# Performance work log

Measured on AMD Instinct MI355X. Metric: run time of the kernel, lower is better.

Reference implementation:

```python
import jax, jax.numpy as jnp
import numpy as np
from jax import lax

B, S, T = 32, 24, 48           # batch, max_num_strokes, max_stroke_len
ENC, SCH, STH = 512, 512, 512  # enc_dim, scene_hdim, stroke_hdim


def _w(k, shape):
    return (jax.random.normal(k, shape, jnp.float32) / np.sqrt(shape[-1])).astype(jnp.float32)


def setup_inputs() -> dict:
    key = jax.random.key(0)
    ks = jax.random.split(key, 12)
    return {
        "enc_features": jax.random.normal(ks[0], (B, ENC), jnp.float32),
        "vector_sketch": jax.random.normal(ks[1], (B, S, T, 5), jnp.float32),
        # force max length == T and num strokes == S so torch's dynamic .max()
        # bounds coincide with the static shapes used here
        "batch_num_strokes": jnp.full((B, 1), S, jnp.int32),
        "batch_stroke_len": jax.random.randint(ks[2], (B, S), 1, T + 1, jnp.int32).at[0, 0].set(T),
        # scene LSTMCell (input = enc_dim + stroke_hdim), torch gate order i,f,g,o
        "W_sc_ih": _w(ks[3], (4 * SCH, ENC + STH)),
        "W_sc_hh": _w(ks[4], (4 * SCH, SCH)),
        "b_sc": jnp.zeros((4 * SCH,), jnp.float32),  # b_ih + b_hh folded
        # stroke LSTM layer 0 (input = scene_hdim + 5)
        "W0_ih": _w(ks[5], (4 * STH, SCH + 5)),
        "W0_hh": _w(ks[6], (4 * STH, STH)),
        "b0": jnp.zeros((4 * STH,), jnp.float32),
        # stroke LSTM layer 1 (input = stroke_hdim)
        "W1_ih": _w(ks[7], (4 * STH, STH)),
        "W1_hh": _w(ks[8], (4 * STH, STH)),
        "b1": jnp.zeros((4 * STH,), jnp.float32),
        # linear_output: stroke_hdim -> 5
        "W_out": _w(ks[9], (5, STH)),
        "b_out": jnp.zeros((5,), jnp.float32),
    }


def _lstm_cell(x, h, c, Wih, Whh, b):
    g = x @ Wih.T + h @ Whh.T + b
    i, f, gg, o = jnp.split(g, 4, axis=-1)
    c = jax.nn.sigmoid(f) * c + jax.nn.sigmoid(i) * jnp.tanh(gg)
    return jax.nn.sigmoid(o) * jnp.tanh(c), c


def _forward(enc_features, vector_sketch, W_sc_ih, W_sc_hh, b_sc, W0_ih, W0_hh, b0,
             W1_ih, W1_hh, b1, W_out, b_out, batch_stroke_len):
    nb = enc_features.shape[0]
    zs = jnp.zeros((nb, SCH), jnp.float32)
    init_tok0 = jnp.tile(jnp.array([[0., 0., 1., 0., 0.]], jnp.float32), (nb, 1))
    t_idx = jnp.arange(T + 1)

    def stroke_step(carry, xs):
        scene_h, scene_c, prev_tok, init_tok = carry
        sketch_s, lens_s = xs                       # (B,T,5), (B,)
        ctx = jnp.concatenate([enc_features, prev_tok], axis=-1)
        scene_h2, scene_c2 = _lstm_cell(ctx, scene_h, scene_c, W_sc_ih, W_sc_hh, b_sc)
        coords = jnp.concatenate([init_tok[:, None, :], sketch_s], axis=1)  # (B,T+1,5)
        lengths = lens_s + 1                        # pack lengths

        def time_step(c2, xt):
            h0, c0, h1, c1 = c2
            x_t, t = xt
            m = (t < lengths)[:, None]              # packed-sequence validity mask
            h0n, c0n = _lstm_cell(jnp.concatenate([scene_h2, x_t], axis=-1), h0, c0, W0_ih, W0_hh, b0)
            h1n, c1n = _lstm_cell(h0n, h1, c1, W1_ih, W1_hh, b1)
            h0 = jnp.where(m, h0n, h0); c0 = jnp.where(m, c0n, c0)
            h1 = jnp.where(m, h1n, h1); c1 = jnp.where(m, c1n, c1)
            return (h0, c0, h1, c1), jnp.where(m, h1, 0.0)  # pad_packed zero-pads outputs

        z = jnp.zeros((nb, STH), jnp.float32)
        (_, _, h1f, _), outs = lax.scan(time_step, (z, z, z, z), (jnp.swapaxes(coords, 0, 1), t_idx))
        # linear applied AFTER zero-padding, so padded-but-within-L steps get the bias (matches torch)
        out_coords = jnp.swapaxes(outs, 0, 1) @ W_out.T + b_out      # (B,T+1,5)
        L = jnp.max(lens_s)
        valid = (jnp.arange(T) < L)[None, :, None]
        stroke_out = jnp.where(valid, out_coords[:, :T, :], 0.0)     # (B,T,5)
        prev_tok = lax.stop_gradient(h1f)          # .detach() in torch
        last = jnp.clip(lens_s - 1, 0, None)
        init_tok2 = jnp.take_along_axis(sketch_s, last[:, None, None], axis=1)[:, 0, :]
        return (scene_h2, scene_c2, prev_tok, init_tok2), stroke_out

    xs = (jnp.swapaxes(vector_sketch, 0, 1), batch_stroke_len.T)     # (S,B,T,5), (S,B)
    _, outs = lax.scan(stroke_step, (zs, zs, zs, init_tok0), xs)
    return jnp.transpose(outs, (1, 0, 2, 3))       # (B,S,T,5)


def reference(enc_features, vector_sketch, batch_num_strokes, batch_stroke_len,
              W_sc_ih, W_sc_hh, b_sc, W0_ih, W0_hh, b0, W1_ih, W1_hh, b1, W_out, b_out):
    # batch_num_strokes only sets the (static) stroke loop bound S
    del batch_num_strokes
    return _forward(enc_features, vector_sketch, W_sc_ih, W_sc_hh, b_sc, W0_ih, W0_hh,
                    b0, W1_ih, W1_hh, b1, W_out, b_out, batch_stroke_len)
```

## Files before the change

kernel.cpp:

```cpp
#include <hip/hip_runtime.h>

#define NB 256
#define NT 256
#define AGT __HIP_MEMORY_SCOPE_AGENT
typedef unsigned long long ull;
typedef _Float16 f16;
typedef __attribute__((ext_vector_type(8))) _Float16 f16x8;
typedef __attribute__((ext_vector_type(4))) float f32x4;
typedef __attribute__((ext_vector_type(4))) unsigned u32x4;


#define BSTR 1056

struct __align__(16) SMem {
  unsigned short Bt[2][2][4 * 528];
  float X[2][4][8];
  int sLens[2][4];
  int sLmax[2];
};

__device__ __forceinline__ float sigm(float x) { return 1.0f / (1.0f + expf(-x)); }
__device__ __forceinline__ unsigned short f16b(float x) {
  union { _Float16 h; unsigned short u; } q; q.h = (_Float16)x; return q.u;
}
__device__ __forceinline__ ull pk4(float a, float b, float c, float d) {
  union { _Float16 h; unsigned short u; } q;
  ull r; q.h = (_Float16)a; r = q.u; q.h = (_Float16)b; r |= (ull)q.u << 16;
  q.h = (_Float16)c; r |= (ull)q.u << 32; q.h = (_Float16)d; r |= (ull)q.u << 48;
  return r;
}
__device__ __forceinline__ u32x4 ld1x16(const void* p) {
  u32x4 r;
  asm volatile("global_load_dwordx4 %0, %1, off sc0 sc1\ns_waitcnt vmcnt(0)"
               : "=&v"(r) : "v"(p) : "memory");
  return r;
}

extern "C" __global__ void __launch_bounds__(NT, 1)
rnn_decoder_kernel(const float* __restrict__ enc, const float* __restrict__ sketch,
                   const int* __restrict__ slen,
                   const float* __restrict__ Wsc_ih, const float* __restrict__ Wsc_hh,
                   const float* __restrict__ bsc,
                   const float* __restrict__ W0ih, const float* __restrict__ W0hh,
                   const float* __restrict__ b0,
                   const float* __restrict__ W1ih, const float* __restrict__ W1hh,
                   const float* __restrict__ b1,
                   const float* __restrict__ Wout, const float* __restrict__ bout,
                   float* __restrict__ out, float* __restrict__ ws)
{
  extern __shared__ char smraw[];
  SMem* sm = (SMem*)smraw;
  const int tid = threadIdx.x;
  const int w = blockIdx.x;
  const int team = w >> 5, slot = w & 31;
  const int lane = tid & 63;
  const int wq = tid >> 6;
  const int l15 = lane & 15;
  const int kq = lane >> 4;
  const int my_b = l15 & 3;
  const int my_u = wq * 4 + kq;

  ull* tb = (ull*)ws + (size_t)team * 6144;
  ull* h0T = tb;
  ull* h1T = tb + 2048;
  ull* sHg = tb + 4096;

  auto grow = [&](int r) { return ((r & 3) << 9) + slot * 16 + (r >> 2); };

  auto ldsB = [&](const unsigned short* Bp, int st) -> f16x8 {
    return *(const f16x8*)((const char*)Bp + my_b * BSTR + st * 64 + kq * 16);
  };
  auto mfma_gv = [&](const float* W, int stride, int coloff, const unsigned short* Bp, f32x4& acc) {
    const float* rp = W + (size_t)grow(wq * 16 + l15) * stride + coloff;
#pragma unroll
    for (int st = 0; st < 16; ++st) {
      const float* q = rp + st * 32 + kq * 8;
      float4 u0 = *(const float4*)q, u1 = *(const float4*)(q + 4);
      f16x8 a;
      a[0] = (f16)u0.x; a[1] = (f16)u0.y; a[2] = (f16)u0.z; a[3] = (f16)u0.w;
      a[4] = (f16)u1.x; a[5] = (f16)u1.y; a[6] = (f16)u1.z; a[7] = (f16)u1.w;
      acc = __builtin_amdgcn_mfma_f32_16x16x32_f16(a, ldsB(Bp, st), acc, 0, 0, 0);
    }
  };
  auto mfma_gs = [&](const float* W, const unsigned short* Bp, f32x4& acc) {
    const float* rp = W + (size_t)grow(wq * 16 + l15) * 517;
#pragma unroll
    for (int st = 0; st < 16; ++st) {
      const float* q = rp + st * 32 + kq * 8;
      f16x8 a;
#pragma unroll
      for (int j = 0; j < 8; ++j) a[j] = (f16)q[j];
      acc = __builtin_amdgcn_mfma_f32_16x16x32_f16(a, ldsB(Bp, st), acc, 0, 0, 0);
    }
  };

  auto putB = [&](unsigned short* Bp, int p, const u32x4& v) {
    int bb2 = p >> 7, up = (2 * p) & 255;
    *(ull*)((char*)Bp + bb2 * BSTR + up * 4) = (ull)v.x | ((ull)v.z << 32);
  };
  auto stageT = [&](const ull* s0, unsigned e0, unsigned short* Bp) {
    const char* p0 = (const char*)s0 + tid * 16;
    const char* p1 = (const char*)s0 + (tid + 256) * 16;
    u32x4 a, b;
    asm volatile("global_load_dwordx4 %0, %2, off sc0 sc1\n"
                 "global_load_dwordx4 %1, %3, off sc0 sc1\n"
                 "s_waitcnt vmcnt(0)"
                 : "=&v"(a), "=&v"(b) : "v"(p0), "v"(p1) : "memory");
    int spins = 0;
    while (((a.y ^ e0) | (a.w ^ e0) | (b.y ^ e0) | (b.w ^ e0)) != 0) {
      if (++spins > 20000) break;
      if (spins > 16) __builtin_amdgcn_s_sleep(1);
      if ((a.y ^ e0) | (a.w ^ e0)) a = ld1x16(p0);
      if ((b.y ^ e0) | (b.w ^ e0)) b = ld1x16(p1);
    }
    putB(Bp, tid, a); putB(Bp, tid + 256, b);
  };

  f16x8 w0hh[16], w1ih[16], whh[16];
  {
    const float* r0 = W0hh + (size_t)grow(wq * 16 + l15) * 512;
    const float* r1 = W1ih + (size_t)grow(wq * 16 + l15) * 512;
    const float* r2 = W1hh + (size_t)grow(wq * 16 + l15) * 512;
#pragma unroll
    for (int st = 0; st < 16; ++st) {
      const int o = st * 32 + kq * 8;
      float4 u0, u1;
      f16x8 a;
      u0 = *(const float4*)(r0 + o); u1 = *(const float4*)(r0 + o + 4);
      a[0] = (f16)u0.x; a[1] = (f16)u0.y; a[2] = (f16)u0.z; a[3] = (f16)u0.w;
      a[4] = (f16)u1.x; a[5] = (f16)u1.y; a[6] = (f16)u1.z; a[7] = (f16)u1.w;
      w0hh[st] = a;
      u0 = *(const float4*)(r1 + o); u1 = *(const float4*)(r1 + o + 4);
      a[0] = (f16)u0.x; a[1] = (f16)u0.y; a[2] = (f16)u0.z; a[3] = (f16)u0.w;
      a[4] = (f16)u1.x; a[5] = (f16)u1.y; a[6] = (f16)u1.z; a[7] = (f16)u1.w;
      w1ih[st] = a;
      u0 = *(const float4*)(r2 + o); u1 = *(const float4*)(r2 + o + 4);
      a[0] = (f16)u0.x; a[1] = (f16)u0.y; a[2] = (f16)u0.z; a[3] = (f16)u0.w;
      a[4] = (f16)u1.x; a[5] = (f16)u1.y; a[6] = (f16)u1.z; a[7] = (f16)u1.w;
      whh[st] = a;
    }
  }
  float cb0[4], cb1[4], cbsc[4], cwx[4][5];
  {
    int gu = slot * 16 + my_u;
#pragma unroll
    for (int gi = 0; gi < 4; ++gi) {
      int gr = gi * 512 + gu;
      cb0[gi] = b0[gr]; cb1[gi] = b1[gr]; cbsc[gi] = bsc[gr];
#pragma unroll
      for (int j = 0; j < 5; ++j) cwx[gi][j] = W0ih[(size_t)gr * 517 + 512 + j];
    }
  }
  const int b_o = slot / 5, o_o = slot % 5;
  const bool oslot = (slot < 20);
  float wo[8]; float bo_r = 0.f;
  if (oslot && tid < 64) {
    bo_r = bout[o_o];
#pragma unroll
    for (int j = 0; j < 8; ++j) wo[j] = Wout[o_o * 512 + lane * 8 + j];
  }

  f32x4 e0reg = {0.f, 0.f, 0.f, 0.f};
  {
    int b2 = tid >> 6, c8 = tid & 63;
    const float* q = enc + (size_t)(4 * team + b2) * 512 + c8 * 8;
    float4 u0 = *(const float4*)q, u1 = *(const float4*)(q + 4);
    unsigned short* Bp = &sm->Bt[0][0][0];
    *(ull*)((char*)Bp + b2 * BSTR + c8 * 16) = pk4(u0.x, u0.y, u0.z, u0.w);
    *(ull*)((char*)Bp + b2 * BSTR + c8 * 16 + 8) = pk4(u1.x, u1.y, u1.z, u1.w);
    __syncthreads();
    mfma_gv(Wsc_ih, 1024, 0, Bp, e0reg);
  }

  float o_csc = 0.f, o_c0 = 0.f, o_h0 = 0.f, o_c1 = 0.f, o_h1 = 0.f;
  int pp = 0;

  for (int s = 0; s < 24; ++s) {
    const unsigned base = 51u * (unsigned)s;

    pp ^= 1;
    {
      int lv = (tid < 32) ? slen[tid * 24 + s] : 0;
      if (tid < 64) {
#pragma unroll
        for (int o2 = 1; o2 < 64; o2 <<= 1) lv = max(lv, __shfl_xor(lv, o2, 64));
        if (tid == 0) sm->sLmax[s & 1] = lv;
      }
      if (tid < 4) sm->sLens[s & 1][tid] = slen[(4 * team + tid) * 24 + s];
    }
    {
      unsigned short* Bp0 = &sm->Bt[pp][0][0];
      unsigned short* Bp1 = &sm->Bt[pp][1][0];
      if (s > 0) {
        stageT(h1T, base, Bp0);
        stageT(sHg + ((s - 1) & 1) * 1024, base - 50u, Bp1);
      }
      __syncthreads();
      f32x4 asc = {0.f, 0.f, 0.f, 0.f};
      if (s > 0) {
        mfma_gv(Wsc_ih, 1024, 512, Bp0, asc);
        mfma_gv(Wsc_hh, 512, 0, Bp1, asc);
      }
      float g[4];
#pragma unroll
      for (int gi = 0; gi < 4; ++gi) g[gi] = e0reg[gi] + cbsc[gi] + asc[gi];
      float c = sigm(g[1]) * o_csc + sigm(g[0]) * tanhf(g[2]);
      float h = sigm(g[3]) * tanhf(c);
      o_csc = c;
      o_c0 = o_h0 = o_c1 = o_h1 = 0.f;
      float hhi = __shfl_down(h, 16, 64);
      if (((kq & 1) == 0) && (l15 < 4)) {
        int chunk = my_b * 256 + slot * 8 + wq * 2 + (kq >> 1);
        unsigned pay = (unsigned)f16b(h) | ((unsigned)f16b(hhi) << 16);
        __hip_atomic_store(&sHg[(s & 1) * 1024 + chunk],
                           (ull)pay | ((ull)(base + 1u) << 32), __ATOMIC_RELAXED, AGT);
      }
    }

    pp ^= 1;
    f32x4 s0reg = {0.f, 0.f, 0.f, 0.f};
    {
      unsigned short* Bp0 = &sm->Bt[pp][0][0];
      if (tid < 4) {
        float xv[5];
        if (s == 0) { xv[0] = 0.f; xv[1] = 0.f; xv[2] = 1.f; xv[3] = 0.f; xv[4] = 0.f; }
        else {
          int bgl = 4 * team + tid;
          int lp = slen[bgl * 24 + (s - 1)];
          int last = min(max(lp - 1, 0), 47);
          const float* q = sketch + ((bgl * 24 + (s - 1)) * 48 + last) * 5;
#pragma unroll
          for (int j = 0; j < 5; ++j) xv[j] = q[j];
        }
#pragma unroll
        for (int j = 0; j < 5; ++j) sm->X[pp][tid][j] = xv[j];
      }
      stageT(sHg + (s & 1) * 1024, base + 1u, Bp0);
      __syncthreads();
      mfma_gs(W0ih, Bp0, s0reg);
      float g[4];
#pragma unroll
      for (int gi = 0; gi < 4; ++gi) {
        float xd = 0.f;
#pragma unroll
        for (int j = 0; j < 5; ++j) xd += cwx[gi][j] * sm->X[pp][my_b][j];
        g[gi] = s0reg[gi] + cb0[gi] + xd;
      }
      float c = sigm(g[1]) * o_c0 + sigm(g[0]) * tanhf(g[2]);
      o_c0 = c; o_h0 = sigm(g[3]) * tanhf(c);
      float hhi = __shfl_down(o_h0, 16, 64);
      if (((kq & 1) == 0) && (l15 < 4)) {
        int chunk = my_b * 256 + slot * 8 + wq * 2 + (kq >> 1);
        unsigned pay = (unsigned)f16b(o_h0) | ((unsigned)f16b(hhi) << 16);
        __hip_atomic_store(&h0T[chunk],
                           (ull)pay | ((ull)(base + 2u) << 32), __ATOMIC_RELAXED, AGT);
      }
    }

    for (int k = 0; k <= 48; ++k) {
      const bool doL0 = (k < 48), doPrev = (k > 0);
      const unsigned eSeq = base + 2u + (unsigned)k, sSeq = eSeq + 1u;
      pp ^= 1;
      unsigned short* B0p = &sm->Bt[pp][0][0];
      unsigned short* B1p = &sm->Bt[pp][1][0];
      if (doL0 && tid < 4) {
        const float* q = sketch + (((4 * team + tid) * 24 + s) * 48 + k) * 5;
#pragma unroll
        for (int j = 0; j < 5; ++j) sm->X[pp][tid][j] = q[j];
      }
      stageT(h0T + (k & 1) * 1024, eSeq, B0p);
      __syncthreads();

      f32x4 a0 = {0.f, 0.f, 0.f, 0.f}, a1 = {0.f, 0.f, 0.f, 0.f};
#pragma unroll
      for (int st = 0; st < 16; ++st) {
        f16x8 bb = ldsB(B0p, st);
        if (doL0) a0 = __builtin_amdgcn_mfma_f32_16x16x32_f16(w0hh[st], bb, a0, 0, 0, 0);
        a1 = __builtin_amdgcn_mfma_f32_16x16x32_f16(w1ih[st], bb, a1, 0, 0, 0);
      }
      const int Lb = sm->sLens[s & 1][my_b];
      if (doL0) {
        if ((k + 1) <= Lb) {
          float g[4];
#pragma unroll
          for (int gi = 0; gi < 4; ++gi) {
            float xd = 0.f;
#pragma unroll
            for (int j = 0; j < 5; ++j) xd += cwx[gi][j] * sm->X[pp][my_b][j];
            g[gi] = a0[gi] + s0reg[gi] + cb0[gi] + xd;
          }
          float c = sigm(g[1]) * o_c0 + sigm(g[0]) * tanhf(g[2]);
          o_c0 = c; o_h0 = sigm(g[3]) * tanhf(c);
        }
        float hhi0 = __shfl_down(o_h0, 16, 64);
        if (((kq & 1) == 0) && (l15 < 4)) {
          int chunk = my_b * 256 + slot * 8 + wq * 2 + (kq >> 1);
          unsigned p0 = (unsigned)f16b(o_h0) | ((unsigned)f16b(hhi0) << 16);
          __hip_atomic_store(&h0T[((k + 1) & 1) * 1024 + chunk],
                             (ull)p0 | ((ull)sSeq << 32), __ATOMIC_RELAXED, AGT);
        }
      }
      if (doPrev) {
        stageT(h1T + ((k - 1) & 1) * 1024, eSeq, B1p);
        __syncthreads();
#pragma unroll
        for (int st = 0; st < 16; ++st)
          a1 = __builtin_amdgcn_mfma_f32_16x16x32_f16(whh[st], ldsB(B1p, st), a1, 0, 0, 0);
      }
      if (k <= Lb) {
        float g[4];
#pragma unroll
        for (int gi = 0; gi < 4; ++gi) g[gi] = a1[gi] + cb1[gi];
        float c = sigm(g[1]) * o_c1 + sigm(g[0]) * tanhf(g[2]);
        o_c1 = c; o_h1 = sigm(g[3]) * tanhf(c);
      }
      float hhi1 = __shfl_down(o_h1, 16, 64);
      if (((kq & 1) == 0) && (l15 < 4)) {
        int chunk = my_b * 256 + slot * 8 + wq * 2 + (kq >> 1);
        unsigned p1 = (unsigned)f16b(o_h1) | ((unsigned)f16b(hhi1) << 16);
        __hip_atomic_store(&h1T[(k & 1) * 1024 + chunk],
                           (ull)p1 | ((ull)sSeq << 32), __ATOMIC_RELAXED, AGT);
      }

      if (doPrev && oslot && tid < 64) {
        f16x8 hv = *(const f16x8*)((const char*)B1p + b_o * BSTR + lane * 16);
        float sd = 0.f;
#pragma unroll
        for (int j = 0; j < 8; ++j) sd += (float)hv[j] * wo[j];
#pragma unroll
        for (int o2 = 1; o2 < 64; o2 <<= 1) sd += __shfl_xor(sd, o2, 64);
        if (tid == 0) {
          int tt = k - 1;
          float val = 0.f;
          if (tt < sm->sLmax[s & 1])
            val = (tt > sm->sLens[s & 1][b_o]) ? bo_r : (sd + bo_r);
          out[(((4 * team + b_o) * 24 + s) * 48 + tt) * 5 + o_o] = val;
        }
      }
    }
  }
}

extern "C" void kernel_launch(void* const* d_in, const int* in_sizes, int n_in,
                              void* d_out, int out_size, void* d_ws, size_t ws_size,
                              hipStream_t stream) {
  (void)in_sizes; (void)n_in; (void)out_size; (void)ws_size;
  int lds_bytes = 98304;
  hipFuncSetAttribute((const void*)rnn_decoder_kernel,
                      hipFuncAttributeMaxDynamicSharedMemorySize, lds_bytes);
  hipMemsetAsync(d_ws, 0, 8 * 6144 * 8, stream);
  rnn_decoder_kernel<<<dim3(NB), dim3(NT), lds_bytes, stream>>>(
      (const float*)d_in[0],
      (const float*)d_in[1],
      (const int*)d_in[3],
      (const float*)d_in[4],
      (const float*)d_in[5],
      (const float*)d_in[6],
      (const float*)d_in[7],
      (const float*)d_in[8],
      (const float*)d_in[9],
      (const float*)d_in[10],
      (const float*)d_in[11],
      (const float*)d_in[12],
      (const float*)d_in[13],
      (const float*)d_in[14],
      (float*)d_out, (float*)d_ws);
}
```

Before: 4.062 ms.

## Prefetch next-step hidden-state polls and publish layer-0 state before layer-1 MFMAs

The global loads that poll the exchanged h0/h1 state are now issued at the end of the previous timestep, so their latency overlaps the output projection and loop overhead instead of sitting on the critical path. The fused W0hh/W1ih MFMA loop is split so the layer-0 gate math and its h0 store run before the W1ih MFMAs. That lets other blocks see the next h0 sooner. The early loads may return stale sequence tags and fall back to re-polling. The explicit vmcnt waits also depend on the exact order in which loads are issued.

New measurement: 4.523 ms. 11.3% more time.

```diff
diff --git a/kernel.cpp b/kernel.cpp
--- a/kernel.cpp
+++ b/kernel.cpp
@@ -34,6 +34,11 @@
   asm volatile("global_load_dwordx4 %0, %1, off sc0 sc1\ns_waitcnt vmcnt(0)"
                : "=&v"(r) : "v"(p) : "memory");
   return r;
+}
+__device__ __forceinline__ void issue2(const void* p0, const void* p1, u32x4& a, u32x4& b) {
+  asm volatile("global_load_dwordx4 %0, %2, off sc0 sc1\n"
+               "global_load_dwordx4 %1, %3, off sc0 sc1"
+               : "=&v"(a), "=&v"(b) : "v"(p0), "v"(p1) : "memory");
 }
 
 extern "C" __global__ void __launch_bounds__(NT, 1)
@@ -115,6 +120,18 @@
     }
     putB(Bp, tid, a); putB(Bp, tid + 256, b);
   };
+  auto pollB = [&](const ull* s0, unsigned e0, u32x4& a, u32x4& b, unsigned short* Bp) {
+    const char* p0 = (const char*)s0 + tid * 16;
+    const char* p1 = (const char*)s0 + (tid + 256) * 16;
+    int spins = 0;
+    while (((a.y ^ e0) | (a.w ^ e0) | (b.y ^ e0) | (b.w ^ e0)) != 0) {
+      if (++spins > 20000) break;
+      if (spins > 16) __builtin_amdgcn_s_sleep(1);
+      if ((a.y ^ e0) | (a.w ^ e0)) a = ld1x16(p0);
+      if ((b.y ^ e0) | (b.w ^ e0)) b = ld1x16(p1);
+    }
+    putB(Bp, tid, a); putB(Bp, tid + 256, b);
+  };
 
   f16x8 w0hh[16], w1ih[16], whh[16];
   {
@@ -174,6 +191,7 @@
 
   float o_csc = 0.f, o_c0 = 0.f, o_h0 = 0.f, o_c1 = 0.f, o_h1 = 0.f;
   int pp = 0;
+  u32x4 fa = {0,0,0,0}, fb = {0,0,0,0}, fc = {0,0,0,0}, fd = {0,0,0,0};
 
   for (int s = 0; s < 24; ++s) {
     const unsigned base = 51u * (unsigned)s;
@@ -255,6 +273,8 @@
         __hip_atomic_store(&h0T[chunk],
                            (ull)pay | ((ull)(base + 2u) << 32), __ATOMIC_RELAXED, AGT);
       }
+      const char* n0 = (const char*)h0T + tid * 16;
+      issue2(n0, n0 + 4096, fa, fb);
     }
 
     for (int k = 0; k <= 48; ++k) {
@@ -268,18 +288,16 @@
 #pragma unroll
         for (int j = 0; j < 5; ++j) sm->X[pp][tid][j] = q[j];
       }
-      stageT(h0T + (k & 1) * 1024, eSeq, B0p);
+      asm volatile("s_waitcnt vmcnt(0)" : "+v"(fa), "+v"(fb) :: "memory");
+      pollB(h0T + (k & 1) * 1024, eSeq, fa, fb, B0p);
       __syncthreads();
 
       f32x4 a0 = {0.f, 0.f, 0.f, 0.f}, a1 = {0.f, 0.f, 0.f, 0.f};
-#pragma unroll
-      for (int st = 0; st < 16; ++st) {
-        f16x8 bb = ldsB(B0p, st);
-        if (doL0) a0 = __builtin_amdgcn_mfma_f32_16x16x32_f16(w0hh[st], bb, a0, 0, 0, 0);
-        a1 = __builtin_amdgcn_mfma_f32_16x16x32_f16(w1ih[st], bb, a1, 0, 0, 0);
-      }
       const int Lb = sm->sLens[s & 1][my_b];
       if (doL0) {
+#pragma unroll
+        for (int st = 0; st < 16; ++st)
+          a0 = __builtin_amdgcn_mfma_f32_16x16x32_f16(w0hh[st], ldsB(B0p, st), a0, 0, 0, 0);
         if ((k + 1) <= Lb) {
           float g[4];
 #pragma unroll
@@ -300,8 +318,14 @@
                              (ull)p0 | ((ull)sSeq << 32), __ATOMIC_RELAXED, AGT);
         }
       }
+#pragma unroll
+      for (int st = 0; st < 16; ++st)
+        a1 = __builtin_amdgcn_mfma_f32_16x16x32_f16(w1ih[st], ldsB(B0p, st), a1, 0, 0, 0);
+
       if (doPrev) {
-        stageT(h1T + ((k - 1) & 1) * 1024, eSeq, B1p);
+        if (doL0) asm volatile("s_waitcnt vmcnt(1)" : "+v"(fc), "+v"(fd) :: "memory");
+        else      asm volatile("s_waitcnt vmcnt(0)" : "+v"(fc), "+v"(fd) :: "memory");
+        pollB(h1T + ((k - 1) & 1) * 1024, eSeq, fc, fd, B1p);
         __syncthreads();
 #pragma unroll
         for (int st = 0; st < 16; ++st)
@@ -320,6 +344,12 @@
         unsigned p1 = (unsigned)f16b(o_h1) | ((unsigned)f16b(hhi1) << 16);
         __hip_atomic_store(&h1T[(k & 1) * 1024 + chunk],
                            (ull)p1 | ((ull)sSeq << 32), __ATOMIC_RELAXED, AGT);
+      }
+      if (k < 48) {
+        const char* n0 = (const char*)(h0T + ((k + 1) & 1) * 1024) + tid * 16;
+        const char* n1 = (const char*)(h1T + (k & 1) * 1024) + tid * 16;
+        issue2(n0, n0 + 4096, fa, fb);
+        issue2(n1, n1 + 4096, fc, fd);
       }
 
       if (doPrev && oslot && tid < 64) {
```
